# Optimization experiments

Measured on AMD Instinct MI355X. Metric: run time of the kernel, lower is better.

The kernel has to match this reference:

```python
import jax, jax.numpy as jnp
import numpy as np

N, E = 100000, 800000
C_IN, C_OUT, OUT_SIZE = 64, 64, 8


def setup_inputs() -> dict:
    key = jax.random.key(0)
    ks = jax.random.split(key, 20)
    s = 0.05
    def p(k, shape):
        return jax.random.normal(k, shape, jnp.float32) * s
    return {
        "x": jax.random.normal(ks[0], (N, C_IN), jnp.float32),
        "edge_index": jax.random.randint(ks[1], (2, E), 0, N),
        "edge_weight": jax.random.uniform(ks[2], (E,), jnp.float32),
        # GCNConv weights (applied as x @ W), one per gate
        "conv_z_W": p(ks[3], (C_IN, C_OUT)), "conv_z_b": p(ks[4], (C_OUT,)),
        "conv_r_W": p(ks[5], (C_IN, C_OUT)), "conv_r_b": p(ks[6], (C_OUT,)),
        "conv_h_W": p(ks[7], (C_IN, C_OUT)), "conv_h_b": p(ks[8], (C_OUT,)),
        # GRU gate linears: Linear(2*C_OUT, C_OUT)
        "lin_z_W": p(ks[9], (2 * C_OUT, C_OUT)), "lin_z_b": p(ks[10], (C_OUT,)),
        "lin_r_W": p(ks[11], (2 * C_OUT, C_OUT)), "lin_r_b": p(ks[12], (C_OUT,)),
        "lin_h_W": p(ks[13], (2 * C_OUT, C_OUT)), "lin_h_b": p(ks[14], (C_OUT,)),
        # output head Linear(C_OUT, OUT_SIZE)
        "head_W": p(ks[15], (C_OUT, OUT_SIZE)), "head_b": p(ks[16], (OUT_SIZE,)),
    }


def _tgcn_forward(x, edge_index, edge_weight,
                  conv_z_W, conv_z_b, conv_r_W, conv_r_b, conv_h_W, conv_h_b,
                  lin_z_W, lin_z_b, lin_r_W, lin_r_b, lin_h_W, lin_h_b,
                  head_W, head_b):
    n = x.shape[0]
    src, dst = edge_index[0], edge_index[1]
    # GCN normalization with self-loops (fill_value = 1)
    loop = jnp.arange(n)
    src_f = jnp.concatenate([src, loop])
    dst_f = jnp.concatenate([dst, loop])
    ew_f = jnp.concatenate([edge_weight, jnp.ones((n,), x.dtype)])
    deg = jax.ops.segment_sum(ew_f, dst_f, num_segments=n)
    deg_safe = jnp.where(deg > 0, deg, 1.0)
    dinv = jnp.where(deg > 0, jax.lax.rsqrt(deg_safe), 0.0)
    norm = dinv[src_f] * ew_f * dinv[dst_f]  # [E + N]

    def gcn(W, b):
        msg = (x @ W)[src_f] * norm[:, None]          # gather + scale
        return jax.ops.segment_sum(msg, dst_f, num_segments=n) + b  # scatter-add

    H = jnp.zeros((n, conv_z_W.shape[1]), x.dtype)
    Z = jax.nn.sigmoid(jnp.concatenate([gcn(conv_z_W, conv_z_b), H], -1) @ lin_z_W + lin_z_b)
    R = jax.nn.sigmoid(jnp.concatenate([gcn(conv_r_W, conv_r_b), H], -1) @ lin_r_W + lin_r_b)
    H_tilde = jnp.tanh(jnp.concatenate([gcn(conv_h_W, conv_h_b), H * R], -1) @ lin_h_W + lin_h_b)
    H = Z * H + (1.0 - Z) * H_tilde
    return jax.nn.relu(H) @ head_W + head_b


def reference(x, edge_index, edge_weight,
              conv_z_W, conv_z_b, conv_r_W, conv_r_b, conv_h_W, conv_h_b,
              lin_z_W, lin_z_b, lin_r_W, lin_r_b, lin_h_W, lin_h_b,
              head_W, head_b):
    return _tgcn_forward(x, edge_index, edge_weight,
                         conv_z_W, conv_z_b, conv_r_W, conv_r_b, conv_h_W, conv_h_b,
                         lin_z_W, lin_z_b, lin_r_W, lin_r_b, lin_h_W, lin_h_b,
                         head_W, head_b)
```

## Files before the change

kernel.cpp:

```cpp
#include <hip/hip_runtime.h>

#define NN 100000
#define NE 800000
#define C 64
#define NB1 391
#define NTILES 3125
#define MAXDEG 40
#define FXSCALE 16777216.0f
#define CNTSHIFT 40


__global__ void ell_build(const int* __restrict__ src, const int* __restrict__ dst,
                          const float* __restrict__ ew,
                          unsigned long long* __restrict__ packed,
                          int2* __restrict__ ell) {
    int e = blockIdx.x * 256 + threadIdx.x;
    if (e >= NE) return;
    int s = src[e], d = dst[e];
    float w = ew[e];
    unsigned long long fx = (unsigned long long)(w * FXSCALE + 0.5f);
    unsigned long long old = atomicAdd(&packed[d], (1ULL << CNTSHIFT) | fx);
    int pos = (int)(old >> CNTSHIFT);
    if (pos < MAXDEG) ell[d * MAXDEG + pos] = make_int2(s, __float_as_int(w));
}

__global__ void finalize_ell(const unsigned long long* __restrict__ packed,
                             float* __restrict__ dinv) {
    int n = blockIdx.x * 256 + threadIdx.x;
    if (n < NN) {
        float degv = (float)(packed[n] & ((1ULL << CNTSHIFT) - 1)) * (1.0f / FXSCALE);
        dinv[n] = rsqrtf(degv + 1.0f);
    }
}

__global__ __launch_bounds__(256) void gather_ell(
    const float* __restrict__ x, const float* __restrict__ dinv,
    const unsigned long long* __restrict__ packed, const int2* __restrict__ ell,
    float* __restrict__ agg) {
    int t = blockIdx.x * 256 + threadIdx.x;
    int n = t >> 6, c = t & 63;
    if (n >= NN) return;
    float di = dinv[n];
    float acc = x[n * C + c] * di * di;
    int cnt = (int)(packed[n] >> CNTSHIFT);
    if (cnt > MAXDEG) cnt = MAXDEG;
    const int2* base = ell + (size_t)n * MAXDEG;
    int e = 0;
    for (; e + 1 < cnt; e += 2) {
        int2 e0 = base[e], e1 = base[e + 1];
        float n0 = dinv[e0.x] * __int_as_float(e0.y) * di;
        float n1 = dinv[e1.x] * __int_as_float(e1.y) * di;
        acc += x[e0.x * C + c] * n0;
        acc += x[e1.x * C + c] * n1;
    }
    if (e < cnt) {
        int2 e0 = base[e];
        acc += x[e0.x * C + c] * (dinv[e0.x] * __int_as_float(e0.y) * di);
    }
    agg[t] = acc;
}


__global__ void count_deg(const int* __restrict__ dst, const float* __restrict__ ew,
                          float* __restrict__ deg, int* __restrict__ cnt) {
    int e = blockIdx.x * blockDim.x + threadIdx.x;
    if (e < NE) {
        int d = dst[e];
        atomicAdd(&deg[d], ew[e]);
        atomicAdd(&cnt[d], 1);
    }
}

__global__ void scan1(const int* __restrict__ cnt, int* __restrict__ row,
                      int* __restrict__ bsum) {
    __shared__ int s[256];
    int tid = threadIdx.x;
    int gid = blockIdx.x * 256 + tid;
    int v = (gid < NN) ? cnt[gid] : 0;
    s[tid] = v;
    for (int off = 1; off < 256; off <<= 1) {
        __syncthreads();
        int t = (tid >= off) ? s[tid - off] : 0;
        __syncthreads();
        s[tid] += t;
    }
    if (gid < NN) row[gid] = s[tid] - v;
    if (tid == 255) bsum[blockIdx.x] = s[255];
}

__global__ void scan2(const int* __restrict__ bsum, int* __restrict__ bo) {
    __shared__ int s[512];
    int tid = threadIdx.x;
    int v = (tid < NB1) ? bsum[tid] : 0;
    s[tid] = v;
    for (int off = 1; off < 512; off <<= 1) {
        __syncthreads();
        int t = (tid >= off) ? s[tid - off] : 0;
        __syncthreads();
        s[tid] += t;
    }
    if (tid < NB1) bo[tid] = s[tid] - v;
}

__global__ void finalize(int* __restrict__ row, const int* __restrict__ bo,
                         int* __restrict__ cursor, const float* __restrict__ deg,
                         float* __restrict__ dinv) {
    int gid = blockIdx.x * 256 + threadIdx.x;
    if (gid < NN) {
        int r = row[gid] + bo[gid >> 8];
        row[gid] = r;
        cursor[gid] = r;
        dinv[gid] = rsqrtf(deg[gid] + 1.0f);
        if (gid == 0) row[NN] = NE;
    }
}

__global__ void bucket(const int* __restrict__ src, const int* __restrict__ dst,
                       const float* __restrict__ ew, const float* __restrict__ dinv,
                       int* __restrict__ cursor, int2* __restrict__ edata) {
    int e = blockIdx.x * 256 + threadIdx.x;
    if (e < NE) {
        int s = src[e], d = dst[e];
        float nrm = dinv[s] * ew[e] * dinv[d];
        int pos = atomicAdd(&cursor[d], 1);
        edata[pos] = make_int2(s, __float_as_int(nrm));
    }
}

__global__ void gather(const float* __restrict__ x, const float* __restrict__ dinv,
                       const int* __restrict__ row, const int2* __restrict__ edata,
                       float* __restrict__ agg) {
    int t = blockIdx.x * 256 + threadIdx.x;
    int n = t >> 6, c = t & 63;
    if (n >= NN) return;
    float di = dinv[n];
    float acc = x[n * C + c] * di * di;
    int e = row[n], end = row[n + 1];
    for (; e + 1 < end; e += 2) {
        int2 e0 = edata[e], e1 = edata[e + 1];
        acc += x[e0.x * C + c] * __int_as_float(e0.y);
        acc += x[e1.x * C + c] * __int_as_float(e1.y);
    }
    if (e < end) {
        int2 e0 = edata[e];
        acc += x[e0.x * C + c] * __int_as_float(e0.y);
    }
    agg[t] = acc;
}


__global__ void deg_scatter(const int* __restrict__ dst, const float* __restrict__ ew,
                            float* __restrict__ deg) {
    int e = blockIdx.x * blockDim.x + threadIdx.x;
    if (e < NE) atomicAdd(&deg[dst[e]], ew[e]);
}

__global__ void node_init(const float* __restrict__ x, const float* __restrict__ deg,
                          float* __restrict__ dinv, float* __restrict__ agg) {
    int t = blockIdx.x * blockDim.x + threadIdx.x;
    if (t >= NN * C) return;
    int n = t >> 6;
    float d = deg[n] + 1.0f;
    float di = rsqrtf(d);
    if ((t & 63) == 0) dinv[n] = di;
    agg[t] = x[t] * (di * di);
}

__global__ void edge_scatter(const int* __restrict__ src, const int* __restrict__ dst,
                             const float* __restrict__ ew, const float* __restrict__ dinv,
                             const float* __restrict__ x, float* __restrict__ agg) {
    int t = blockIdx.x * blockDim.x + threadIdx.x;
    int e = t >> 6;
    int c = t & 63;
    if (e >= NE) return;
    int s = src[e];
    int d = dst[e];
    float nrm = dinv[s] * ew[e] * dinv[d];
    atomicAdd(&agg[d * C + c], x[s * C + c] * nrm);
}

__global__ void fuse_weights(const float* __restrict__ Wz, const float* __restrict__ bz,
                             const float* __restrict__ Lz, const float* __restrict__ lzb,
                             const float* __restrict__ Wh, const float* __restrict__ bh,
                             const float* __restrict__ Lh, const float* __restrict__ lhb,
                             float* __restrict__ WzF, float* __restrict__ bzF,
                             float* __restrict__ WhF, float* __restrict__ bhF) {
    int t = blockIdx.x * blockDim.x + threadIdx.x;
    if (t < 4096) {
        int i = t >> 6, j = t & 63;
        float s = 0.0f;
#pragma unroll 8
        for (int k = 0; k < 64; k++) s += Wz[i * 64 + k] * Lz[k * 64 + j];
        WzF[t] = s;
    } else if (t < 8192) {
        int u = t - 4096;
        int i = u >> 6, j = u & 63;
        float s = 0.0f;
#pragma unroll 8
        for (int k = 0; k < 64; k++) s += Wh[i * 64 + k] * Lh[k * 64 + j];
        WhF[u] = s;
    } else if (t < 8256) {
        int j = t - 8192;
        float s = lzb[j];
#pragma unroll 8
        for (int k = 0; k < 64; k++) s += bz[k] * Lz[k * 64 + j];
        bzF[j] = s;
    } else if (t < 8320) {
        int j = t - 8256;
        float s = lhb[j];
#pragma unroll 8
        for (int k = 0; k < 64; k++) s += bh[k] * Lh[k * 64 + j];
        bhF[j] = s;
    }
}

__global__ __launch_bounds__(256) void gate_head(
    const float* __restrict__ agg,
    const float* __restrict__ WzF, const float* __restrict__ bzF,
    const float* __restrict__ WhF, const float* __restrict__ bhF,
    const float* __restrict__ headW, const float* __restrict__ headb,
    float* __restrict__ out) {
    __shared__ float sWz[4096];
    __shared__ float sWh[4096];
    __shared__ float sHead[512];
    __shared__ float sbz[64], sbh[64], shb[8];
    __shared__ float sAgg[32][64];
    __shared__ float sRh[32][65];

    int tid = threadIdx.x;
    for (int i = tid; i < 4096; i += 256) { sWz[i] = WzF[i]; sWh[i] = WhF[i]; }
    for (int i = tid; i < 512; i += 256) sHead[i] = headW[i];
    if (tid < 64) { sbz[tid] = bzF[tid]; sbh[tid] = bhF[tid]; }
    if (tid < 8) shb[tid] = headb[tid];
    __syncthreads();

    int j = tid & 63;
    int g = tid >> 6;
    int nl = tid >> 3;
    int j8 = tid & 7;

    for (int tIdx = blockIdx.x; tIdx < NTILES; tIdx += gridDim.x) {
        int n0 = tIdx * 32;
        for (int i = tid; i < 32 * 64; i += 256)
            sAgg[i >> 6][i & 63] = agg[n0 * 64 + i];
        __syncthreads();

        float az[8], ah[8];
#pragma unroll
        for (int l = 0; l < 8; l++) { az[l] = sbz[j]; ah[l] = sbh[j]; }
#pragma unroll 8
        for (int k = 0; k < 64; k++) {
            float wz = sWz[k * 64 + j];
            float wh = sWh[k * 64 + j];
#pragma unroll
            for (int l = 0; l < 8; l++) {
                float a = sAgg[g * 8 + l][k];
                az[l] += a * wz;
                ah[l] += a * wh;
            }
        }
#pragma unroll
        for (int l = 0; l < 8; l++) {
            float z = 1.0f / (1.0f + __expf(-az[l]));
            float ac = fminf(fmaxf(ah[l], -15.0f), 15.0f);
            float e2 = __expf(2.0f * ac);
            float ht = (e2 - 1.0f) / (e2 + 1.0f);
            float h = (1.0f - z) * ht;
            sRh[g * 8 + l][j] = fmaxf(h, 0.0f);
        }
        __syncthreads();

        float s = shb[j8];
#pragma unroll 8
        for (int k = 0; k < 64; k++) s += sRh[nl][k] * sHead[k * 8 + j8];
        out[(n0 + nl) * 8 + j8] = s;
        __syncthreads();
    }
}

extern "C" void kernel_launch(void* const* d_in, const int* in_sizes, int n_in,
                              void* d_out, int out_size, void* d_ws, size_t ws_size,
                              hipStream_t stream) {
    const float* x     = (const float*)d_in[0];
    const int*   ei    = (const int*)d_in[1];
    const float* ew    = (const float*)d_in[2];
    const float* Wz    = (const float*)d_in[3];
    const float* bz    = (const float*)d_in[4];
    const float* Wh    = (const float*)d_in[7];
    const float* bh    = (const float*)d_in[8];
    const float* Lz    = (const float*)d_in[9];
    const float* lzb   = (const float*)d_in[10];
    const float* Lh    = (const float*)d_in[13];
    const float* lhb   = (const float*)d_in[14];
    const float* headW = (const float*)d_in[15];
    const float* headb = (const float*)d_in[16];
    float* out = (float*)d_out;

    const int* src = ei;
    const int* dst = ei + NE;

    float* agg    = (float*)d_ws;
    float* dinv   = agg + (size_t)NN * C;
    float* WzF    = dinv + NN;
    float* WhF    = WzF + 4096;
    float* bzF    = WhF + 4096;
    float* bhF    = bzF + 64;
    float* tail   = bhF + 64;

    unsigned long long* packed = (unsigned long long*)tail;
    int2* ell = (int2*)(packed + NN);
    size_t need_ell = (size_t)(tail - (float*)d_ws) * 4 + (size_t)NN * 8
                    + (size_t)NN * MAXDEG * 8;

    float* deg    = tail;
    int*   cnt    = (int*)(deg + NN);
    int*   row    = cnt + NN;
    int*   cursor = row + NN + 1;
    int*   bsum   = cursor + NN;
    int*   bo     = bsum + 512;
    int2*  edata  = (int2*)(bo + 512 + 1);
    size_t need_csr  = ((size_t)(bo + 512 + 1 - (int*)d_ws) + 2 * (size_t)NE) * 4;
    size_t need_base = (size_t)((int*)cnt - (int*)d_ws) * 4;

    fuse_weights<<<33, 256, 0, stream>>>(Wz, bz, Lz, lzb, Wh, bh, Lh, lhb,
                                         WzF, bzF, WhF, bhF);

    if (ws_size >= need_ell) {
        hipMemsetAsync(packed, 0, NN * sizeof(unsigned long long), stream);
        ell_build<<<(NE + 255) / 256, 256, 0, stream>>>(src, dst, ew, packed, ell);
        finalize_ell<<<NB1, 256, 0, stream>>>(packed, dinv);
        gather_ell<<<(NN * C) / 256, 256, 0, stream>>>(x, dinv, packed, ell, agg);
    } else if (ws_size >= need_csr) {
        hipMemsetAsync(deg, 0, NN * sizeof(float), stream);
        hipMemsetAsync(cnt, 0, NN * sizeof(int), stream);
        count_deg<<<(NE + 255) / 256, 256, 0, stream>>>(dst, ew, deg, cnt);
        scan1<<<NB1, 256, 0, stream>>>(cnt, row, bsum);
        scan2<<<1, 512, 0, stream>>>(bsum, bo);
        finalize<<<NB1, 256, 0, stream>>>(row, bo, cursor, deg, dinv);
        bucket<<<(NE + 255) / 256, 256, 0, stream>>>(src, dst, ew, dinv, cursor, edata);
        gather<<<(NN * C) / 256, 256, 0, stream>>>(x, dinv, row, edata, agg);
    } else if (ws_size >= need_base) {
        hipMemsetAsync(deg, 0, NN * sizeof(float), stream);
        deg_scatter<<<(NE + 255) / 256, 256, 0, stream>>>(dst, ew, deg);
        node_init<<<(NN * C + 255) / 256, 256, 0, stream>>>(x, deg, dinv, agg);
        edge_scatter<<<(NE * C) / 256, 256, 0, stream>>>(src, dst, ew, dinv, x, agg);
    }

    gate_head<<<768, 256, 0, stream>>>(agg, WzF, bzF, WhF, bhF, headW, headb, out);
}
```

Baseline: 258.3 us.

## Fuse ELL gather with gate and head computation in persistent kernel

Merges the ELL neighbor-aggregation kernel with the gated GRU update and output head into one persistent kernel, with one wave per node. The separate gate_head pass and the 100000x64 agg round trip through global memory go away. The edge loop now reads two edges per 16-byte load and unrolls by four. In exchange each block stages about 35KB of weights in LDS, which limits occupancy, and the per-node matvec from shared memory may become the bottleneck.

New measurement: 287.0 us. 1.11x slower.

```diff
diff --git a/kernel.cpp b/kernel.cpp
--- a/kernel.cpp
+++ b/kernel.cpp
@@ -33,31 +33,74 @@
     }
 }
 
-__global__ __launch_bounds__(256) void gather_ell(
+__global__ __launch_bounds__(256) void gather_gate(
     const float* __restrict__ x, const float* __restrict__ dinv,
     const unsigned long long* __restrict__ packed, const int2* __restrict__ ell,
-    float* __restrict__ agg) {
-    int t = blockIdx.x * 256 + threadIdx.x;
-    int n = t >> 6, c = t & 63;
-    if (n >= NN) return;
-    float di = dinv[n];
-    float acc = x[n * C + c] * di * di;
-    int cnt = (int)(packed[n] >> CNTSHIFT);
-    if (cnt > MAXDEG) cnt = MAXDEG;
-    const int2* base = ell + (size_t)n * MAXDEG;
-    int e = 0;
-    for (; e + 1 < cnt; e += 2) {
-        int2 e0 = base[e], e1 = base[e + 1];
-        float n0 = dinv[e0.x] * __int_as_float(e0.y) * di;
-        float n1 = dinv[e1.x] * __int_as_float(e1.y) * di;
-        acc += x[e0.x * C + c] * n0;
-        acc += x[e1.x * C + c] * n1;
-    }
-    if (e < cnt) {
-        int2 e0 = base[e];
-        acc += x[e0.x * C + c] * (dinv[e0.x] * __int_as_float(e0.y) * di);
-    }
-    agg[t] = acc;
+    const float* __restrict__ WzF, const float* __restrict__ bzF,
+    const float* __restrict__ WhF, const float* __restrict__ bhF,
+    const float* __restrict__ headW, const float* __restrict__ headb,
+    float* __restrict__ out) {
+    __shared__ float sWz[4096];
+    __shared__ float sWh[4096];
+    __shared__ float sHead[512];
+    __shared__ float sbz[64], sbh[64], shb[8];
+    __shared__ float sRow[4][64];
+    __shared__ float sH[4][64];
+
+    int tid = threadIdx.x;
+    for (int i = tid; i < 4096; i += 256) { sWz[i] = WzF[i]; sWh[i] = WhF[i]; }
+    for (int i = tid; i < 512; i += 256) sHead[i] = headW[i];
+    if (tid < 64) { sbz[tid] = bzF[tid]; sbh[tid] = bhF[tid]; }
+    if (tid < 8) shb[tid] = headb[tid];
+    __syncthreads();
+
+    int w = tid >> 6, c = tid & 63;
+    int nwaves = gridDim.x * 4;
+    for (int n = blockIdx.x * 4 + w; n < NN; n += nwaves) {
+        float di = dinv[n];
+        float acc = x[n * C + c] * di * di;
+        int cnt = (int)(packed[n] >> CNTSHIFT);
+        if (cnt > MAXDEG) cnt = MAXDEG;
+        const int2* base = ell + (size_t)n * MAXDEG;
+        int e = 0;
+        for (; e + 3 < cnt; e += 4) {
+            int4 q0 = *(const int4*)(base + e);
+            int4 q1 = *(const int4*)(base + e + 2);
+            float d0 = dinv[q0.x], d1 = dinv[q0.z], d2 = dinv[q1.x], d3 = dinv[q1.z];
+            float x0 = x[q0.x * C + c], x1 = x[q0.z * C + c];
+            float x2 = x[q1.x * C + c], x3 = x[q1.z * C + c];
+            acc += x0 * (d0 * __int_as_float(q0.y) * di);
+            acc += x1 * (d1 * __int_as_float(q0.w) * di);
+            acc += x2 * (d2 * __int_as_float(q1.y) * di);
+            acc += x3 * (d3 * __int_as_float(q1.w) * di);
+        }
+        for (; e < cnt; ++e) {
+            int2 e0 = base[e];
+            acc += x[e0.x * C + c] * (dinv[e0.x] * __int_as_float(e0.y) * di);
+        }
+        sRow[w][c] = acc;
+
+        float az = sbz[c], ah = sbh[c];
+#pragma unroll 8
+        for (int k = 0; k < 64; k++) {
+            float a = sRow[w][k];
+            az += a * sWz[k * 64 + c];
+            ah += a * sWh[k * 64 + c];
+        }
+        float z = 1.0f / (1.0f + __expf(-az));
+        float ac2 = fminf(fmaxf(ah, -15.0f), 15.0f);
+        float e2 = __expf(2.0f * ac2);
+        float ht = (e2 - 1.0f) / (e2 + 1.0f);
+        float h = (1.0f - z) * ht;
+        sH[w][c] = fmaxf(h, 0.0f);
+
+        if (c < 8) {
+            float s = shb[c];
+#pragma unroll 8
+            for (int k = 0; k < 64; k++) s += sH[w][k] * sHead[k * 8 + c];
+            out[n * 8 + c] = s;
+        }
+    }
 }
 
 
@@ -329,7 +372,8 @@
         hipMemsetAsync(packed, 0, NN * sizeof(unsigned long long), stream);
         ell_build<<<(NE + 255) / 256, 256, 0, stream>>>(src, dst, ew, packed, ell);
         finalize_ell<<<NB1, 256, 0, stream>>>(packed, dinv);
-        gather_ell<<<(NN * C) / 256, 256, 0, stream>>>(x, dinv, packed, ell, agg);
+        gather_gate<<<2048, 256, 0, stream>>>(x, dinv, packed, ell,
+                                              WzF, bzF, WhF, bhF, headW, headb, out);
     } else if (ws_size >= need_csr) {
         hipMemsetAsync(deg, 0, NN * sizeof(float), stream);
         hipMemsetAsync(cnt, 0, NN * sizeof(int), stream);
@@ -339,12 +383,12 @@
         finalize<<<NB1, 256, 0, stream>>>(row, bo, cursor, deg, dinv);
         bucket<<<(NE + 255) / 256, 256, 0, stream>>>(src, dst, ew, dinv, cursor, edata);
         gather<<<(NN * C) / 256, 256, 0, stream>>>(x, dinv, row, edata, agg);
+        gate_head<<<768, 256, 0, stream>>>(agg, WzF, bzF, WhF, bhF, headW, headb, out);
     } else if (ws_size >= need_base) {
         hipMemsetAsync(deg, 0, NN * sizeof(float), stream);
         deg_scatter<<<(NE + 255) / 256, 256, 0, stream>>>(dst, ew, deg);
         node_init<<<(NN * C + 255) / 256, 256, 0, stream>>>(x, deg, dinv, agg);
         edge_scatter<<<(NE * C) / 256, 256, 0, stream>>>(src, dst, ew, dinv, x, agg);
-    }
-
-    gate_head<<<768, 256, 0, stream>>>(agg, WzF, bzF, WhF, bhF, headW, headb, out);
-}
+        gate_head<<<768, 256, 0, stream>>>(agg, WzF, bzF, WhF, bhF, headW, headb, out);
+    }
+}
```

## Pack ELL entries into 32-bit src|15-bit weight and unroll gather by eight

Applied to the files above, without the earlier changes.

Each ELL entry shrinks from an int2 (src, float weight) to one 32-bit word holding the source index shifted by 15 bits plus a 15-bit fixed-point weight. The 64-bit packed count/degree atomic becomes a 32-bit count atomic, and degrees are recomputed in finalize_ell with a wave reduction over each node's ELL row. gather_ell now loads entries with uint4 vectors and unrolls by eight to issue more independent loads at once. This halves ELL traffic, but quantizing weights to 15 bits costs accuracy. Packing also requires node indices below 2^17, which holds for N=100000.

New measurement: 255.8 us. Within noise of the previous version (-0.9%).

```diff
diff --git a/kernel.cpp b/kernel.cpp
--- a/kernel.cpp
+++ b/kernel.cpp
@@ -6,56 +6,81 @@
 #define NB1 391
 #define NTILES 3125
 #define MAXDEG 40
-#define FXSCALE 16777216.0f
-#define CNTSHIFT 40
+#define WBITS 15
+#define WMASK 32767u
+#define WSCALE 32768.0f
 
 
 __global__ void ell_build(const int* __restrict__ src, const int* __restrict__ dst,
                           const float* __restrict__ ew,
-                          unsigned long long* __restrict__ packed,
-                          int2* __restrict__ ell) {
+                          unsigned* __restrict__ cnt, unsigned* __restrict__ ell) {
     int e = blockIdx.x * 256 + threadIdx.x;
     if (e >= NE) return;
     int s = src[e], d = dst[e];
     float w = ew[e];
-    unsigned long long fx = (unsigned long long)(w * FXSCALE + 0.5f);
-    unsigned long long old = atomicAdd(&packed[d], (1ULL << CNTSHIFT) | fx);
-    int pos = (int)(old >> CNTSHIFT);
-    if (pos < MAXDEG) ell[d * MAXDEG + pos] = make_int2(s, __float_as_int(w));
-}
-
-__global__ void finalize_ell(const unsigned long long* __restrict__ packed,
+    unsigned w15 = (unsigned)(w * WSCALE + 0.5f);
+    if (w15 > WMASK) w15 = WMASK;
+    unsigned pos = atomicAdd(&cnt[d], 1u);
+    if (pos < MAXDEG) ell[d * MAXDEG + pos] = ((unsigned)s << WBITS) | w15;
+}
+
+__global__ void finalize_ell(const unsigned* __restrict__ cnt,
+                             const unsigned* __restrict__ ell,
                              float* __restrict__ dinv) {
-    int n = blockIdx.x * 256 + threadIdx.x;
-    if (n < NN) {
-        float degv = (float)(packed[n] & ((1ULL << CNTSHIFT) - 1)) * (1.0f / FXSCALE);
-        dinv[n] = rsqrtf(degv + 1.0f);
-    }
+    int t = blockIdx.x * 256 + threadIdx.x;
+    int n = t >> 6, l = t & 63;
+    if (n >= NN) return;
+    int k = min((int)cnt[n], MAXDEG);
+    float w = (l < k) ? (float)(ell[n * MAXDEG + l] & WMASK) * (1.0f / WSCALE) : 0.0f;
+    for (int off = 32; off; off >>= 1) w += __shfl_xor(w, off, 64);
+    if (l == 0) dinv[n] = rsqrtf(w + 1.0f);
 }
 
 __global__ __launch_bounds__(256) void gather_ell(
     const float* __restrict__ x, const float* __restrict__ dinv,
-    const unsigned long long* __restrict__ packed, const int2* __restrict__ ell,
+    const unsigned* __restrict__ cnt, const unsigned* __restrict__ ell,
     float* __restrict__ agg) {
     int t = blockIdx.x * 256 + threadIdx.x;
     int n = t >> 6, c = t & 63;
     if (n >= NN) return;
     float di = dinv[n];
     float acc = x[n * C + c] * di * di;
-    int cnt = (int)(packed[n] >> CNTSHIFT);
-    if (cnt > MAXDEG) cnt = MAXDEG;
-    const int2* base = ell + (size_t)n * MAXDEG;
+    int k = min((int)cnt[n], MAXDEG);
+    const unsigned* base = ell + (size_t)n * MAXDEG;
     int e = 0;
-    for (; e + 1 < cnt; e += 2) {
-        int2 e0 = base[e], e1 = base[e + 1];
-        float n0 = dinv[e0.x] * __int_as_float(e0.y) * di;
-        float n1 = dinv[e1.x] * __int_as_float(e1.y) * di;
-        acc += x[e0.x * C + c] * n0;
-        acc += x[e1.x * C + c] * n1;
-    }
-    if (e < cnt) {
-        int2 e0 = base[e];
-        acc += x[e0.x * C + c] * (dinv[e0.x] * __int_as_float(e0.y) * di);
+    for (; e + 7 < k; e += 8) {
+        uint4 q0 = *(const uint4*)(base + e);
+        uint4 q1 = *(const uint4*)(base + e + 4);
+        int s0 = q0.x >> WBITS, s1 = q0.y >> WBITS, s2 = q0.z >> WBITS, s3 = q0.w >> WBITS;
+        int s4 = q1.x >> WBITS, s5 = q1.y >> WBITS, s6 = q1.z >> WBITS, s7 = q1.w >> WBITS;
+        float x0 = x[s0 * C + c], x1 = x[s1 * C + c], x2 = x[s2 * C + c], x3 = x[s3 * C + c];
+        float x4 = x[s4 * C + c], x5 = x[s5 * C + c], x6 = x[s6 * C + c], x7 = x[s7 * C + c];
+        float d0 = dinv[s0], d1 = dinv[s1], d2 = dinv[s2], d3 = dinv[s3];
+        float d4 = dinv[s4], d5 = dinv[s5], d6 = dinv[s6], d7 = dinv[s7];
+        acc += x0 * (d0 * (float)(q0.x & WMASK) * (di * (1.0f / WSCALE)));
+        acc += x1 * (d1 * (float)(q0.y & WMASK) * (di * (1.0f / WSCALE)));
+        acc += x2 * (d2 * (float)(q0.z & WMASK) * (di * (1.0f / WSCALE)));
+        acc += x3 * (d3 * (float)(q0.w & WMASK) * (di * (1.0f / WSCALE)));
+        acc += x4 * (d4 * (float)(q1.x & WMASK) * (di * (1.0f / WSCALE)));
+        acc += x5 * (d5 * (float)(q1.y & WMASK) * (di * (1.0f / WSCALE)));
+        acc += x6 * (d6 * (float)(q1.z & WMASK) * (di * (1.0f / WSCALE)));
+        acc += x7 * (d7 * (float)(q1.w & WMASK) * (di * (1.0f / WSCALE)));
+    }
+    if (e + 3 < k) {
+        uint4 q0 = *(const uint4*)(base + e);
+        int s0 = q0.x >> WBITS, s1 = q0.y >> WBITS, s2 = q0.z >> WBITS, s3 = q0.w >> WBITS;
+        float x0 = x[s0 * C + c], x1 = x[s1 * C + c], x2 = x[s2 * C + c], x3 = x[s3 * C + c];
+        float d0 = dinv[s0], d1 = dinv[s1], d2 = dinv[s2], d3 = dinv[s3];
+        acc += x0 * (d0 * (float)(q0.x & WMASK) * (di * (1.0f / WSCALE)));
+        acc += x1 * (d1 * (float)(q0.y & WMASK) * (di * (1.0f / WSCALE)));
+        acc += x2 * (d2 * (float)(q0.z & WMASK) * (di * (1.0f / WSCALE)));
+        acc += x3 * (d3 * (float)(q0.w & WMASK) * (di * (1.0f / WSCALE)));
+        e += 4;
+    }
+    for (; e < k; ++e) {
+        unsigned u = base[e];
+        int s = u >> WBITS;
+        acc += x[s * C + c] * (dinv[s] * (float)(u & WMASK) * (di * (1.0f / WSCALE)));
     }
     agg[t] = acc;
 }
@@ -146,37 +171,6 @@
         acc += x[e0.x * C + c] * __int_as_float(e0.y);
     }
     agg[t] = acc;
-}
-
-
-__global__ void deg_scatter(const int* __restrict__ dst, const float* __restrict__ ew,
-                            float* __restrict__ deg) {
-    int e = blockIdx.x * blockDim.x + threadIdx.x;
-    if (e < NE) atomicAdd(&deg[dst[e]], ew[e]);
-}
-
-__global__ void node_init(const float* __restrict__ x, const float* __restrict__ deg,
-                          float* __restrict__ dinv, float* __restrict__ agg) {
-    int t = blockIdx.x * blockDim.x + threadIdx.x;
-    if (t >= NN * C) return;
-    int n = t >> 6;
-    float d = deg[n] + 1.0f;
-    float di = rsqrtf(d);
-    if ((t & 63) == 0) dinv[n] = di;
-    agg[t] = x[t] * (di * di);
-}
-
-__global__ void edge_scatter(const int* __restrict__ src, const int* __restrict__ dst,
-                             const float* __restrict__ ew, const float* __restrict__ dinv,
-                             const float* __restrict__ x, float* __restrict__ agg) {
-    int t = blockIdx.x * blockDim.x + threadIdx.x;
-    int e = t >> 6;
-    int c = t & 63;
-    if (e >= NE) return;
-    int s = src[e];
-    int d = dst[e];
-    float nrm = dinv[s] * ew[e] * dinv[d];
-    atomicAdd(&agg[d * C + c], x[s * C + c] * nrm);
 }
 
 __global__ void fuse_weights(const float* __restrict__ Wz, const float* __restrict__ bz,
@@ -278,6 +272,37 @@
     }
 }
 
+
+__global__ void deg_scatter(const int* __restrict__ dst, const float* __restrict__ ew,
+                            float* __restrict__ deg) {
+    int e = blockIdx.x * blockDim.x + threadIdx.x;
+    if (e < NE) atomicAdd(&deg[dst[e]], ew[e]);
+}
+
+__global__ void node_init(const float* __restrict__ x, const float* __restrict__ deg,
+                          float* __restrict__ dinv, float* __restrict__ agg) {
+    int t = blockIdx.x * blockDim.x + threadIdx.x;
+    if (t >= NN * C) return;
+    int n = t >> 6;
+    float d = deg[n] + 1.0f;
+    float di = rsqrtf(d);
+    if ((t & 63) == 0) dinv[n] = di;
+    agg[t] = x[t] * (di * di);
+}
+
+__global__ void edge_scatter(const int* __restrict__ src, const int* __restrict__ dst,
+                             const float* __restrict__ ew, const float* __restrict__ dinv,
+                             const float* __restrict__ x, float* __restrict__ agg) {
+    int t = blockIdx.x * blockDim.x + threadIdx.x;
+    int e = t >> 6;
+    int c = t & 63;
+    if (e >= NE) return;
+    int s = src[e];
+    int d = dst[e];
+    float nrm = dinv[s] * ew[e] * dinv[d];
+    atomicAdd(&agg[d * C + c], x[s * C + c] * nrm);
+}
+
 extern "C" void kernel_launch(void* const* d_in, const int* in_sizes, int n_in,
                               void* d_out, int out_size, void* d_ws, size_t ws_size,
                               hipStream_t stream) {
@@ -307,10 +332,10 @@
     float* bhF    = bzF + 64;
     float* tail   = bhF + 64;
 
-    unsigned long long* packed = (unsigned long long*)tail;
-    int2* ell = (int2*)(packed + NN);
-    size_t need_ell = (size_t)(tail - (float*)d_ws) * 4 + (size_t)NN * 8
-                    + (size_t)NN * MAXDEG * 8;
+    unsigned* cnt_u = (unsigned*)tail;
+    unsigned* ell   = cnt_u + NN;
+    size_t need_ell = (size_t)(tail - (float*)d_ws) * 4 + (size_t)NN * 4
+                    + (size_t)NN * MAXDEG * 4;
 
     float* deg    = tail;
     int*   cnt    = (int*)(deg + NN);
@@ -326,10 +351,11 @@
                                          WzF, bzF, WhF, bhF);
 
     if (ws_size >= need_ell) {
-        hipMemsetAsync(packed, 0, NN * sizeof(unsigned long long), stream);
-        ell_build<<<(NE + 255) / 256, 256, 0, stream>>>(src, dst, ew, packed, ell);
-        finalize_ell<<<NB1, 256, 0, stream>>>(packed, dinv);
-        gather_ell<<<(NN * C) / 256, 256, 0, stream>>>(x, dinv, packed, ell, agg);
+        hipMemsetAsync(cnt_u, 0, NN * sizeof(unsigned), stream);
+        ell_build<<<(NE + 255) / 256, 256, 0, stream>>>(src, dst, ew, cnt_u, ell);
+        finalize_ell<<<(NN * 64 + 255) / 256, 256, 0, stream>>>(cnt_u, ell, dinv);
+        gather_ell<<<(NN * C) / 256, 256, 0, stream>>>(x, dinv, cnt_u, ell, agg);
+        gate_head<<<768, 256, 0, stream>>>(agg, WzF, bzF, WhF, bhF, headW, headb, out);
     } else if (ws_size >= need_csr) {
         hipMemsetAsync(deg, 0, NN * sizeof(float), stream);
         hipMemsetAsync(cnt, 0, NN * sizeof(int), stream);
@@ -339,12 +365,12 @@
         finalize<<<NB1, 256, 0, stream>>>(row, bo, cursor, deg, dinv);
         bucket<<<(NE + 255) / 256, 256, 0, stream>>>(src, dst, ew, dinv, cursor, edata);
         gather<<<(NN * C) / 256, 256, 0, stream>>>(x, dinv, row, edata, agg);
+        gate_head<<<768, 256, 0, stream>>>(agg, WzF, bzF, WhF, bhF, headW, headb, out);
     } else if (ws_size >= need_base) {
         hipMemsetAsync(deg, 0, NN * sizeof(float), stream);
         deg_scatter<<<(NE + 255) / 256, 256, 0, stream>>>(dst, ew, deg);
         node_init<<<(NN * C + 255) / 256, 256, 0, stream>>>(x, deg, dinv, agg);
         edge_scatter<<<(NE * C) / 256, 256, 0, stream>>>(src, dst, ew, dinv, x, agg);
-    }
-
-    gate_head<<<768, 256, 0, stream>>>(agg, WzF, bzF, WhF, bhF, headW, headb, out);
-}
+        gate_head<<<768, 256, 0, stream>>>(agg, WzF, bzF, WhF, bhF, headW, headb, out);
+    }
+}
```
